# Kernel tuning notes

Measured on AMD Instinct MI355X. Metric: run time of the kernel, lower is better.

## Reference

```python
import jax, jax.numpy as jnp
import numpy as np
import math

VOCAB = 32000
HIDDEN = 256
N_HEADS = 8
HEAD_DIM = 32
MAX_LEN = 2048


def _pos_encoding(max_len, d_model, dtype=jnp.float32):
    # Matches PositionalEncoding buffer (even d_model).
    pos = jnp.arange(max_len, dtype=dtype)[:, None]                       # [L,1]
    div = jnp.exp(jnp.arange(0, d_model, 2, dtype=dtype) * (-(math.log(10000.0) / d_model)))
    ang = pos * div                                                        # [L, d/2]
    pe = jnp.zeros((max_len, d_model), dtype=dtype)
    pe = pe.at[:, 0::2].set(jnp.sin(ang))
    pe = pe.at[:, 1::2].set(jnp.cos(ang))
    return pe


def setup_inputs() -> dict:
    key = jax.random.key(0)
    ks = jax.random.split(key, 7)
    B, S = 8, 2047
    s = 0.02
    x = jax.random.randint(ks[0], (B, S), 0, VOCAB + 1, dtype=jnp.int64)
    emb_w = jax.random.normal(ks[1], (VOCAB + 1, HIDDEN), jnp.float32) * s
    wq = jax.random.normal(ks[2], (N_HEADS, HEAD_DIM, HIDDEN), jnp.float32) * s
    wk = jax.random.normal(ks[3], (N_HEADS, HEAD_DIM, HIDDEN), jnp.float32) * s
    wv = jax.random.normal(ks[4], (N_HEADS, HEAD_DIM, HIDDEN), jnp.float32) * s
    wo = jax.random.normal(ks[5], (HIDDEN, N_HEADS * HEAD_DIM), jnp.float32) * s
    wu = jax.random.normal(ks[6], (VOCAB + 1, HIDDEN), jnp.float32) * s
    return {"x": x, "emb_w": emb_w, "wq": wq, "wk": wk, "wv": wv, "wo": wo, "wu": wu}


def reference(x, emb_w, wq, wk, wv, wo, wu):
    B, S = x.shape
    # prepend CLS token (id=2)
    tok = jnp.concatenate([jnp.full((B, 1), 2, dtype=x.dtype), x], axis=1)  # [B, S+1]
    y = emb_w[tok]                                                          # [B, S+1, H]
    y = y + _pos_encoding(S + 1, HIDDEN, y.dtype)
    # batched per-head QKV (nn.Linear: out = in @ W.T)
    q = jnp.einsum('bsh,nkh->bnsk', y, wq)
    k = jnp.einsum('bsh,nkh->bnsk', y, wk)
    v = jnp.einsum('bsh,nkh->bnsk', y, wv)
    scores = jnp.einsum('bnsk,bntk->bnst', q, k) / (HEAD_DIM ** 0.5)        # [B,N,S+1,S+1]
    A = jax.nn.softmax(scores, axis=-1)
    o = jnp.einsum('bnst,bntk->bnsk', A, v)                                 # [B,N,S+1,K]
    o = jnp.transpose(o, (0, 2, 1, 3)).reshape(B, S + 1, N_HEADS * HEAD_DIM)
    att = o @ wo.T + y     # residual inside MultiHeadAttention
    y = att + y            # second residual in MultiHeadTransformerPosEmb.forward
    out = y[:, 0, :] @ wu.T                                                 # [B, VOCAB+1]
    return out
```

## Files before the change

kernel.cpp:

```cpp
#include <hip/hip_runtime.h>
#include <stdint.h>

#define B_   8
#define S_   2047
#define L_   2048
#define H_   256
#define NH_  8
#define HD_  32
#define V_   32001
#define GRID_ 2048
#define BAR_STRIDE_ 2048

__device__ __forceinline__ void ast(float* p, float v) {
    __hip_atomic_store((unsigned int*)p, __float_as_uint(v),
                       __ATOMIC_RELAXED, __HIP_MEMORY_SCOPE_AGENT);
}
__device__ __forceinline__ float ald(const float* p) {
    return __uint_as_float(__hip_atomic_load((const unsigned int*)p,
                           __ATOMIC_RELAXED, __HIP_MEMORY_SCOPE_AGENT));
}
__device__ __forceinline__ unsigned aadd(unsigned* p) {
    return __hip_atomic_fetch_add(p, 1u, __ATOMIC_RELAXED, __HIP_MEMORY_SCOPE_AGENT);
}
__device__ __forceinline__ unsigned aldu(const unsigned* p) {
    return __hip_atomic_load(p, __ATOMIC_RELAXED, __HIP_MEMORY_SCOPE_AGENT);
}
__device__ __forceinline__ void vdrain() {
    asm volatile("s_waitcnt vmcnt(0)" ::: "memory");
}
__device__ __forceinline__ float foldx(float a, int off) {
    return a + __shfl_xor(a, off, 64);
}

__device__ __forceinline__ void gsync(unsigned int* bp, int bid) {
    __syncthreads();
    if (threadIdx.x == 0) {
        int sg = bid & 31;
        unsigned int* sub = bp + 16 + sg * 16;
        unsigned int* rel = bp + 528 + sg * 16;
        unsigned int prev = aadd(sub);
        if (prev == (GRID_ / 32) - 1) {
            unsigned int m = aadd(bp);
            if (m == 31u) {
                for (int i = 0; i < 32; ++i)
                    __hip_atomic_store(bp + 528 + i * 16, 1u,
                                       __ATOMIC_RELAXED, __HIP_MEMORY_SCOPE_AGENT);
            }
        }
        while (aldu(rel) == 0u) __builtin_amdgcn_s_sleep(2);
    }
    __syncthreads();
}

__global__ __launch_bounds__(256, 8) void mega(const int* __restrict__ x,
                                               const float* __restrict__ emb,
                                               const float* __restrict__ wq,
                                               const float* __restrict__ wk,
                                               const float* __restrict__ wv,
                                               const float* __restrict__ wo,
                                               const float* __restrict__ wu,
                                               float* __restrict__ out,
                                               float* __restrict__ qk,
                                               float* __restrict__ z,
                                               float* __restrict__ obar,
                                               float* __restrict__ ebar,
                                               float* __restrict__ esum,
                                               float* __restrict__ psum,
                                               unsigned int* __restrict__ bars) {
    int bid = blockIdx.x, tid = threadIdx.x;
    int lane = tid & 63, w = tid >> 6;

    __shared__ float sm[4200];

    if (bid < NH_) {
        int n = bid;
        float* y0l = sm;
        float* q0p = sm + 256;
        float* q0l = sm + 512;
        float v = emb[2 * H_ + tid] + ((tid & 1) ? 1.0f : 0.0f);
        y0l[tid] = v;
        __syncthreads();
        {
            int k = tid >> 3, part = tid & 7;
            const float* wr = wq + (n * HD_ + k) * H_ + part * 32;
            const float* yy = y0l + part * 32;
            float acc = 0.f;
#pragma unroll
            for (int j = 0; j < 32; ++j) acc += wr[j] * yy[j];
            q0p[k * 8 + part] = acc;
        }
        __syncthreads();
        if (tid < HD_) {
            float s = 0.f;
#pragma unroll
            for (int j = 0; j < 8; ++j) s += q0p[tid * 8 + j];
            q0l[tid] = s;
        }
        __syncthreads();
        float acc = 0.f;
        for (int k = 0; k < HD_; ++k)
            acc += q0l[k] * wk[(n * HD_ + k) * H_ + tid];
        ast(qk + n * H_ + tid, acc * 0.17677669529663687f);
    }
    vdrain();
    gsync(bars + 0 * BAR_STRIDE_, bid);

    {
        int b = bid >> 8, c = bid & 255;
        int h0 = lane * 4;
        float* qk_l = sm;
        float* y4_l = sm + 2048;
        float* e_l  = sm + 4096;

        for (int i = tid; i < NH_ * H_; i += 256) qk_l[i] = ald(qk + i);
        __syncthreads();

        const float cdiv = 0.07195578414202881f;
        float div0 = __expf(-(float)(lane * 2) * cdiv);
        float div1 = __expf(-(float)(lane * 2 + 1) * cdiv);

#pragma unroll
        for (int it = 0; it < 2; ++it) {
            int tl = w * 2 + it;
            int t = c * 8 + tl;
            int tok = (t == 0) ? 2 : x[b * S_ + t - 1];
            float4 ev = *(const float4*)(emb + (size_t)tok * H_ + h0);
            float a0 = (float)t * div0, a1 = (float)t * div1;
            float4 y4;
            y4.x = ev.x + __sinf(a0); y4.y = ev.y + __cosf(a0);
            y4.z = ev.z + __sinf(a1); y4.w = ev.w + __cosf(a1);
            *(float4*)&y4_l[tl * 256 + h0] = y4;

            float a[NH_];
#pragma unroll
            for (int n = 0; n < NH_; ++n) {
                float4 q4 = *(const float4*)&qk_l[n * H_ + h0];
                a[n] = q4.x * y4.x + q4.y * y4.y + q4.z * y4.z + q4.w * y4.w;
            }
            float m4[4];
#pragma unroll
            for (int k = 0; k < 4; ++k) {
                float lo = foldx(a[k], 32), hi = foldx(a[k + 4], 32);
                m4[k] = (lane & 32) ? hi : lo;
            }
            float m2[2];
#pragma unroll
            for (int k = 0; k < 2; ++k) {
                float lo = foldx(m4[k], 16), hi = foldx(m4[k + 2], 16);
                m2[k] = (lane & 16) ? hi : lo;
            }
            float lo = foldx(m2[0], 8), hi = foldx(m2[1], 8);
            float m1 = (lane & 8) ? hi : lo;
            m1 = foldx(m1, 4); m1 = foldx(m1, 2); m1 = foldx(m1, 1);
            float e = __expf(m1);
            if ((lane & 7) == 0) e_l[tl * 8 + (lane >> 3)] = e;
        }
        __syncthreads();

        int n0 = w * 2, n1 = n0 + 1;
        float4 A0 = make_float4(0.f, 0.f, 0.f, 0.f);
        float4 A1 = make_float4(0.f, 0.f, 0.f, 0.f);
        float es0 = 0.f, es1 = 0.f;
#pragma unroll
        for (int tl = 0; tl < 8; ++tl) {
            float4 yv = *(const float4*)&y4_l[tl * 256 + h0];
            float e0 = e_l[tl * 8 + n0];
            float e1 = e_l[tl * 8 + n1];
            A0.x += e0 * yv.x; A0.y += e0 * yv.y; A0.z += e0 * yv.z; A0.w += e0 * yv.w;
            A1.x += e1 * yv.x; A1.y += e1 * yv.y; A1.z += e1 * yv.z; A1.w += e1 * yv.w;
            es0 += e0; es1 += e1;
        }
        float* p0 = psum + (size_t)bid * (NH_ * H_) + n0 * H_ + h0;
        ast(p0 + 0, A0.x); ast(p0 + 1, A0.y); ast(p0 + 2, A0.z); ast(p0 + 3, A0.w);
        float* p1 = psum + (size_t)bid * (NH_ * H_) + n1 * H_ + h0;
        ast(p1 + 0, A1.x); ast(p1 + 1, A1.y); ast(p1 + 2, A1.z); ast(p1 + 3, A1.w);
        if (lane == 0) {
            ast(esum + bid * NH_ + n0, es0);
            ast(esum + bid * NH_ + n1, es1);
        }
    }
    vdrain();
    gsync(bars + 1 * BAR_STRIDE_, bid);

    {
        int b = bid >> 8, jg = bid & 255;
        int jl = tid & 7, c8 = tid >> 3;
        int j = jg * 8 + jl;
        float s = 0.f;
#pragma unroll
        for (int i = 0; i < 8; ++i)
            s += ald(psum + (size_t)(b * 256 + c8 * 8 + i) * (NH_ * H_) + j);
        sm[jl * 32 + c8] = s;
        __syncthreads();
        if (tid < 8) {
            float t = 0.f;
#pragma unroll
            for (int g = 0; g < 32; ++g) t += sm[tid * 32 + g];
            ast(obar + b * (NH_ * H_) + jg * 8 + tid, t);
        }
        if (jg == 0) {
            int n = tid & 7;
            float e = 0.f;
#pragma unroll
            for (int i = 0; i < 8; ++i)
                e += ald(esum + (b * 256 + c8 * 8 + i) * NH_ + n);
            sm[256 + n * 32 + c8] = e;
            __syncthreads();
            if (tid < 8) {
                float t = 0.f;
#pragma unroll
                for (int g = 0; g < 32; ++g) t += sm[256 + tid * 32 + g];
                ast(ebar + b * NH_ + tid, t);
            }
        }
    }
    vdrain();
    gsync(bars + 2 * BAR_STRIDE_, bid);

    if (bid < B_) {
        int b = bid;
        float* ybar_l = sm;
        float* o_l    = sm + 2048;
        float* sB     = sm + 2304;
        if (tid < NH_) sB[tid] = 1.0f / ald(ebar + b * NH_ + tid);
        __syncthreads();
        for (int i = tid; i < NH_ * H_; i += 256)
            ybar_l[i] = ald(obar + b * (NH_ * H_) + i) * sB[i >> 8];
        __syncthreads();
        {
            int n = tid >> 5;
            const float* wrow = wv + (size_t)tid * H_;
            const float* yy = ybar_l + n * H_;
            float s = 0.f;
#pragma unroll 16
            for (int j4 = 0; j4 < H_ / 4; ++j4) {
                float4 w4 = *(const float4*)(wrow + j4 * 4);
                s += w4.x * yy[j4 * 4] + w4.y * yy[j4 * 4 + 1]
                   + w4.z * yy[j4 * 4 + 2] + w4.w * yy[j4 * 4 + 3];
            }
            o_l[tid] = s;
        }
        __syncthreads();
        {
            float y0v = emb[2 * H_ + tid] + ((tid & 1) ? 1.0f : 0.0f);
            const float* wrow = wo + (size_t)tid * (NH_ * HD_);
            float s = 0.f;
#pragma unroll 16
            for (int j4 = 0; j4 < (NH_ * HD_) / 4; ++j4) {
                float4 w4 = *(const float4*)(wrow + j4 * 4);
                s += w4.x * o_l[j4 * 4] + w4.y * o_l[j4 * 4 + 1]
                   + w4.z * o_l[j4 * 4 + 2] + w4.w * o_l[j4 * 4 + 3];
            }
            ast(z + b * H_ + tid, s + 2.0f * y0v);
        }
    }
    vdrain();
    gsync(bars + 3 * BAR_STRIDE_, bid);

    if (bid < (V_ + 15) / 16) {
        int m = lane & 15, g = lane >> 4;
        int base = bid * 16;
        float* zs = sm;
        float* sm_out = sm + 2560;
        for (int i = tid; i < B_ * H_; i += 256) {
            int bb = i >> 8, h = i & 255;
            zs[bb * 320 + (h >> 4) * 20 + (h & 15)] = ald(z + i);
        }
        __syncthreads();

        int rl = w * 4 + g;
        int v = base + rl;
        int vc = (v < V_) ? v : (V_ - 1);
        const float* wr = wu + (size_t)vc * H_ + m * 16;
        float4 w0 = *(const float4*)(wr);
        float4 w1 = *(const float4*)(wr + 4);
        float4 w2 = *(const float4*)(wr + 8);
        float4 w3 = *(const float4*)(wr + 12);
        float acc[B_];
#pragma unroll
        for (int bb = 0; bb < B_; ++bb) {
            const float* zb = zs + bb * 320 + m * 20;
            float4 z0 = *(const float4*)(zb);
            float4 z1 = *(const float4*)(zb + 4);
            float4 z2 = *(const float4*)(zb + 8);
            float4 z3 = *(const float4*)(zb + 12);
            acc[bb] = z0.x * w0.x + z0.y * w0.y + z0.z * w0.z + z0.w * w0.w
                    + z1.x * w1.x + z1.y * w1.y + z1.z * w1.z + z1.w * w1.w
                    + z2.x * w2.x + z2.y * w2.y + z2.z * w2.z + z2.w * w2.w
                    + z3.x * w3.x + z3.y * w3.y + z3.z * w3.z + z3.w * w3.w;
        }
#pragma unroll
        for (int off = 1; off <= 8; off <<= 1) {
#pragma unroll
            for (int bb = 0; bb < B_; ++bb) acc[bb] += __shfl_xor(acc[bb], off, 64);
        }
        if (m < B_) {
            float v8 = acc[0];
            v8 = (m == 1) ? acc[1] : v8;
            v8 = (m == 2) ? acc[2] : v8;
            v8 = (m == 3) ? acc[3] : v8;
            v8 = (m == 4) ? acc[4] : v8;
            v8 = (m == 5) ? acc[5] : v8;
            v8 = (m == 6) ? acc[6] : v8;
            v8 = (m == 7) ? acc[7] : v8;
            sm_out[m * 17 + rl] = v8;
        }
        __syncthreads();
        if (tid < B_ * 16) {
            int bb = tid >> 4, vl = tid & 15, vv = base + vl;
            if (vv < V_) out[bb * V_ + vv] = sm_out[bb * 17 + vl];
        }
    }
}

extern "C" void kernel_launch(void* const* d_in, const int* in_sizes, int n_in,
                              void* d_out, int out_size, void* d_ws, size_t ws_size,
                              hipStream_t stream) {
    const int*   x   = (const int*)d_in[0];
    const float* emb = (const float*)d_in[1];
    const float* wq  = (const float*)d_in[2];
    const float* wk  = (const float*)d_in[3];
    const float* wv  = (const float*)d_in[4];
    const float* wo  = (const float*)d_in[5];
    const float* wu  = (const float*)d_in[6];
    float*       out = (float*)d_out;

    float* qk   = (float*)d_ws;
    float* z    = qk + NH_ * H_;
    float* obar = z + B_ * H_;
    float* ebar = obar + B_ * NH_ * H_;
    float* esum = ebar + B_ * NH_;
    float* psum = esum + (size_t)GRID_ * NH_;
    unsigned int* bars = (unsigned int*)(psum + (size_t)GRID_ * NH_ * H_);

    hipMemsetAsync(bars, 0, 4 * BAR_STRIDE_ * sizeof(unsigned int), stream);

    mega<<<GRID_, 256, 0, stream>>>(x, emb, wq, wk, wv, wo, wu, out,
                                    qk, z, obar, ebar, esum, psum, bars);
}
```

Measured before the change: 169.8 us.

## Halve persistent grid to 1024 blocks with 16-token chunks per block

Cuts the persistent megakernel grid from 2048 to 1024 blocks. Each block now handles 16 tokens instead of 8, and the attention dot products are recomputed as a per-thread (token, head, half) partial reduction in shared memory instead of a shuffle tree. The psum reduction stage and the final vocab projection are re-partitioned to match: each block does 32 vocab rows in two passes. The aim is cheaper grid-wide barriers and less partial-sum traffic, at the cost of more work per block and lower occupancy (launch bounds drop from 8 to 4).

```diff
diff --git a/kernel.cpp b/kernel.cpp
--- a/kernel.cpp
+++ b/kernel.cpp
@@ -8,8 +8,11 @@
 #define NH_  8
 #define HD_  32
 #define V_   32001
-#define GRID_ 2048
+#define NCH_ 128
+#define TCH_ 16
+#define GRID_ 1024
 #define BAR_STRIDE_ 2048
+#define YP_  260
 
 __device__ __forceinline__ void ast(float* p, float v) {
     __hip_atomic_store((unsigned int*)p, __float_as_uint(v),
@@ -28,8 +31,16 @@
 __device__ __forceinline__ void vdrain() {
     asm volatile("s_waitcnt vmcnt(0)" ::: "memory");
 }
-__device__ __forceinline__ float foldx(float a, int off) {
-    return a + __shfl_xor(a, off, 64);
+__device__ __forceinline__ float sel8(const float a[8], int j) {
+    float v = a[0];
+    v = (j == 1) ? a[1] : v;
+    v = (j == 2) ? a[2] : v;
+    v = (j == 3) ? a[3] : v;
+    v = (j == 4) ? a[4] : v;
+    v = (j == 5) ? a[5] : v;
+    v = (j == 6) ? a[6] : v;
+    v = (j == 7) ? a[7] : v;
+    return v;
 }
 
 __device__ __forceinline__ void gsync(unsigned int* bp, int bid) {
@@ -52,7 +63,7 @@
     __syncthreads();
 }
 
-__global__ __launch_bounds__(256, 8) void mega(const int* __restrict__ x,
+__global__ __launch_bounds__(256, 4) void mega(const int* __restrict__ x,
                                                const float* __restrict__ emb,
                                                const float* __restrict__ wq,
                                                const float* __restrict__ wk,
@@ -70,7 +81,7 @@
     int bid = blockIdx.x, tid = threadIdx.x;
     int lane = tid & 63, w = tid >> 6;
 
-    __shared__ float sm[4200];
+    __shared__ float sm[6640];
 
     if (bid < NH_) {
         int n = bid;
@@ -106,110 +117,108 @@
     gsync(bars + 0 * BAR_STRIDE_, bid);
 
     {
-        int b = bid >> 8, c = bid & 255;
-        int h0 = lane * 4;
-        float* qk_l = sm;
-        float* y4_l = sm + 2048;
-        float* e_l  = sm + 4096;
-
-        for (int i = tid; i < NH_ * H_; i += 256) qk_l[i] = ald(qk + i);
+        int b = bid >> 7, c = bid & 127;
+        int t0 = c * TCH_;
+        float* y_l   = sm;
+        float* qk_l  = sm + TCH_ * YP_;
+        float* e_l   = qk_l + NH_ * YP_;
+        float* part  = e_l + TCH_ * NH_;
+        __shared__ int tok_l[TCH_];
+
+        if (tid < TCH_) {
+            int t = t0 + tid;
+            tok_l[tid] = (t == 0) ? 2 : x[b * S_ + t - 1];
+        }
+        for (int i = tid; i < NH_ * H_; i += 256)
+            qk_l[(i >> 8) * YP_ + (i & 255)] = ald(qk + i);
         __syncthreads();
 
         const float cdiv = 0.07195578414202881f;
-        float div0 = __expf(-(float)(lane * 2) * cdiv);
-        float div1 = __expf(-(float)(lane * 2 + 1) * cdiv);
-
-#pragma unroll
-        for (int it = 0; it < 2; ++it) {
-            int tl = w * 2 + it;
-            int t = c * 8 + tl;
-            int tok = (t == 0) ? 2 : x[b * S_ + t - 1];
-            float4 ev = *(const float4*)(emb + (size_t)tok * H_ + h0);
-            float a0 = (float)t * div0, a1 = (float)t * div1;
-            float4 y4;
-            y4.x = ev.x + __sinf(a0); y4.y = ev.y + __cosf(a0);
-            y4.z = ev.z + __sinf(a1); y4.w = ev.w + __cosf(a1);
-            *(float4*)&y4_l[tl * 256 + h0] = y4;
-
-            float a[NH_];
-#pragma unroll
-            for (int n = 0; n < NH_; ++n) {
-                float4 q4 = *(const float4*)&qk_l[n * H_ + h0];
-                a[n] = q4.x * y4.x + q4.y * y4.y + q4.z * y4.z + q4.w * y4.w;
-            }
-            float m4[4];
-#pragma unroll
-            for (int k = 0; k < 4; ++k) {
-                float lo = foldx(a[k], 32), hi = foldx(a[k + 4], 32);
-                m4[k] = (lane & 32) ? hi : lo;
-            }
-            float m2[2];
-#pragma unroll
-            for (int k = 0; k < 2; ++k) {
-                float lo = foldx(m4[k], 16), hi = foldx(m4[k + 2], 16);
-                m2[k] = (lane & 16) ? hi : lo;
-            }
-            float lo = foldx(m2[0], 8), hi = foldx(m2[1], 8);
-            float m1 = (lane & 8) ? hi : lo;
-            m1 = foldx(m1, 4); m1 = foldx(m1, 2); m1 = foldx(m1, 1);
-            float e = __expf(m1);
-            if ((lane & 7) == 0) e_l[tl * 8 + (lane >> 3)] = e;
-        }
-        __syncthreads();
-
-        int n0 = w * 2, n1 = n0 + 1;
-        float4 A0 = make_float4(0.f, 0.f, 0.f, 0.f);
-        float4 A1 = make_float4(0.f, 0.f, 0.f, 0.f);
-        float es0 = 0.f, es1 = 0.f;
-#pragma unroll
-        for (int tl = 0; tl < 8; ++tl) {
-            float4 yv = *(const float4*)&y4_l[tl * 256 + h0];
-            float e0 = e_l[tl * 8 + n0];
-            float e1 = e_l[tl * 8 + n1];
-            A0.x += e0 * yv.x; A0.y += e0 * yv.y; A0.z += e0 * yv.z; A0.w += e0 * yv.w;
-            A1.x += e1 * yv.x; A1.y += e1 * yv.y; A1.z += e1 * yv.z; A1.w += e1 * yv.w;
-            es0 += e0; es1 += e1;
-        }
-        float* p0 = psum + (size_t)bid * (NH_ * H_) + n0 * H_ + h0;
-        ast(p0 + 0, A0.x); ast(p0 + 1, A0.y); ast(p0 + 2, A0.z); ast(p0 + 3, A0.w);
-        float* p1 = psum + (size_t)bid * (NH_ * H_) + n1 * H_ + h0;
-        ast(p1 + 0, A1.x); ast(p1 + 1, A1.y); ast(p1 + 2, A1.z); ast(p1 + 3, A1.w);
-        if (lane == 0) {
-            ast(esum + bid * NH_ + n0, es0);
-            ast(esum + bid * NH_ + n1, es1);
+        float divc = __expf(-(float)(tid >> 1) * cdiv);
+        bool isOdd = (tid & 1);
+#pragma unroll 4
+        for (int r = 0; r < TCH_; ++r) {
+            int t = t0 + r;
+            float ev = emb[(size_t)tok_l[r] * H_ + tid];
+            float ang = (float)t * divc;
+            float pe = isOdd ? __cosf(ang) : __sinf(ang);
+            y_l[r * YP_ + tid] = ev + pe;
+        }
+        __syncthreads();
+
+        {
+            int half = tid >> 7, tn = tid & 127;
+            int t = tn >> 3, n = tn & 7;
+            const float* yr = y_l + t * YP_ + half * 128;
+            const float* qr = qk_l + n * YP_ + half * 128;
+            float s = 0.f;
+#pragma unroll
+            for (int j = 0; j < 32; ++j) {
+                float4 y4 = *(const float4*)(yr + j * 4);
+                float4 q4 = *(const float4*)(qr + j * 4);
+                s += y4.x * q4.x + y4.y * q4.y + y4.z * q4.z + y4.w * q4.w;
+            }
+            part[tid] = s;
+        }
+        __syncthreads();
+        if (tid < 128)
+            e_l[tid] = __expf(part[tid] + part[128 + tid]);
+        __syncthreads();
+
+        {
+            float acc[NH_] = {};
+#pragma unroll
+            for (int t = 0; t < TCH_; ++t) {
+                float yv = y_l[t * YP_ + tid];
+                float4 eA = *(const float4*)&e_l[t * 8];
+                float4 eB = *(const float4*)&e_l[t * 8 + 4];
+                acc[0] += eA.x * yv; acc[1] += eA.y * yv;
+                acc[2] += eA.z * yv; acc[3] += eA.w * yv;
+                acc[4] += eB.x * yv; acc[5] += eB.y * yv;
+                acc[6] += eB.z * yv; acc[7] += eB.w * yv;
+            }
+#pragma unroll
+            for (int n = 0; n < NH_; ++n)
+                ast(psum + (size_t)bid * (NH_ * H_) + n * H_ + tid, acc[n]);
+        }
+        if (tid < NH_) {
+            float s = 0.f;
+#pragma unroll
+            for (int t = 0; t < TCH_; ++t) s += e_l[t * 8 + tid];
+            ast(esum + bid * NH_ + tid, s);
         }
     }
     vdrain();
     gsync(bars + 1 * BAR_STRIDE_, bid);
 
     {
-        int b = bid >> 8, jg = bid & 255;
-        int jl = tid & 7, c8 = tid >> 3;
-        int j = jg * 8 + jl;
+        int b = bid >> 7, jg = bid & 127;
+        int jl = tid & 15, cg = tid >> 4;
+        int j = jg * 16 + jl;
         float s = 0.f;
 #pragma unroll
         for (int i = 0; i < 8; ++i)
-            s += ald(psum + (size_t)(b * 256 + c8 * 8 + i) * (NH_ * H_) + j);
-        sm[jl * 32 + c8] = s;
-        __syncthreads();
-        if (tid < 8) {
+            s += ald(psum + (size_t)(b * NCH_ + cg * 8 + i) * (NH_ * H_) + j);
+        sm[cg * 16 + jl] = s;
+        __syncthreads();
+        if (tid < 16) {
             float t = 0.f;
 #pragma unroll
-            for (int g = 0; g < 32; ++g) t += sm[tid * 32 + g];
-            ast(obar + b * (NH_ * H_) + jg * 8 + tid, t);
+            for (int g = 0; g < 16; ++g) t += sm[g * 16 + tid];
+            ast(obar + b * (NH_ * H_) + jg * 16 + tid, t);
         }
         if (jg == 0) {
-            int n = tid & 7;
+            int n = tid & 7, cg2 = tid >> 3;
             float e = 0.f;
 #pragma unroll
-            for (int i = 0; i < 8; ++i)
-                e += ald(esum + (b * 256 + c8 * 8 + i) * NH_ + n);
-            sm[256 + n * 32 + c8] = e;
+            for (int i = 0; i < 4; ++i)
+                e += ald(esum + (b * NCH_ + cg2 * 4 + i) * NH_ + n);
+            sm[512 + cg2 * 8 + n] = e;
             __syncthreads();
             if (tid < 8) {
                 float t = 0.f;
 #pragma unroll
-                for (int g = 0; g < 32; ++g) t += sm[256 + tid * 32 + g];
+                for (int g = 0; g < 32; ++g) t += sm[512 + g * 8 + tid];
                 ast(ebar + b * NH_ + tid, t);
             }
         }
@@ -257,9 +266,9 @@
     vdrain();
     gsync(bars + 3 * BAR_STRIDE_, bid);
 
-    if (bid < (V_ + 15) / 16) {
+    if (bid < (V_ + 31) / 32) {
         int m = lane & 15, g = lane >> 4;
-        int base = bid * 16;
+        int base = bid * 32;
         float* zs = sm;
         float* sm_out = sm + 2560;
         for (int i = tid; i < B_ * H_; i += 256) {
@@ -268,47 +277,41 @@
         }
         __syncthreads();
 
-        int rl = w * 4 + g;
-        int v = base + rl;
-        int vc = (v < V_) ? v : (V_ - 1);
-        const float* wr = wu + (size_t)vc * H_ + m * 16;
-        float4 w0 = *(const float4*)(wr);
-        float4 w1 = *(const float4*)(wr + 4);
-        float4 w2 = *(const float4*)(wr + 8);
-        float4 w3 = *(const float4*)(wr + 12);
-        float acc[B_];
-#pragma unroll
-        for (int bb = 0; bb < B_; ++bb) {
-            const float* zb = zs + bb * 320 + m * 20;
-            float4 z0 = *(const float4*)(zb);
-            float4 z1 = *(const float4*)(zb + 4);
-            float4 z2 = *(const float4*)(zb + 8);
-            float4 z3 = *(const float4*)(zb + 12);
-            acc[bb] = z0.x * w0.x + z0.y * w0.y + z0.z * w0.z + z0.w * w0.w
-                    + z1.x * w1.x + z1.y * w1.y + z1.z * w1.z + z1.w * w1.w
-                    + z2.x * w2.x + z2.y * w2.y + z2.z * w2.z + z2.w * w2.w
-                    + z3.x * w3.x + z3.y * w3.y + z3.z * w3.z + z3.w * w3.w;
-        }
-#pragma unroll
-        for (int off = 1; off <= 8; off <<= 1) {
-#pragma unroll
-            for (int bb = 0; bb < B_; ++bb) acc[bb] += __shfl_xor(acc[bb], off, 64);
-        }
-        if (m < B_) {
-            float v8 = acc[0];
-            v8 = (m == 1) ? acc[1] : v8;
-            v8 = (m == 2) ? acc[2] : v8;
-            v8 = (m == 3) ? acc[3] : v8;
-            v8 = (m == 4) ? acc[4] : v8;
-            v8 = (m == 5) ? acc[5] : v8;
-            v8 = (m == 6) ? acc[6] : v8;
-            v8 = (m == 7) ? acc[7] : v8;
-            sm_out[m * 17 + rl] = v8;
-        }
-        __syncthreads();
-        if (tid < B_ * 16) {
-            int bb = tid >> 4, vl = tid & 15, vv = base + vl;
-            if (vv < V_) out[bb * V_ + vv] = sm_out[bb * 17 + vl];
+#pragma unroll
+        for (int pass = 0; pass < 2; ++pass) {
+            int rl = pass * 16 + w * 4 + g;
+            int v = base + rl;
+            int vc = (v < V_) ? v : (V_ - 1);
+            const float* wr = wu + (size_t)vc * H_ + m * 16;
+            float4 w0 = *(const float4*)(wr);
+            float4 w1 = *(const float4*)(wr + 4);
+            float4 w2 = *(const float4*)(wr + 8);
+            float4 w3 = *(const float4*)(wr + 12);
+            float acc[B_];
+#pragma unroll
+            for (int bb = 0; bb < B_; ++bb) {
+                const float* zb = zs + bb * 320 + m * 20;
+                float4 z0 = *(const float4*)(zb);
+                float4 z1 = *(const float4*)(zb + 4);
+                float4 z2 = *(const float4*)(zb + 8);
+                float4 z3 = *(const float4*)(zb + 12);
+                acc[bb] = z0.x * w0.x + z0.y * w0.y + z0.z * w0.z + z0.w * w0.w
+                        + z1.x * w1.x + z1.y * w1.y + z1.z * w1.z + z1.w * w1.w
+                        + z2.x * w2.x + z2.y * w2.y + z2.z * w2.z + z2.w * w2.w
+                        + z3.x * w3.x + z3.y * w3.y + z3.z * w3.z + z3.w * w3.w;
+            }
+#pragma unroll
+            for (int off = 1; off <= 8; off <<= 1) {
+#pragma unroll
+                for (int bb = 0; bb < B_; ++bb)
+                    acc[bb] += __shfl_xor(acc[bb], off, 64);
+            }
+            if (m < B_) sm_out[m * 33 + rl] = sel8(acc, m);
+        }
+        __syncthreads();
+        {
+            int bb = tid >> 5, vl = tid & 31, vv = base + vl;
+            if (vv < V_) out[bb * V_ + vv] = sm_out[bb * 33 + vl];
         }
     }
 }
```

After: 150.1 us. -11.6%, faster.
